# Optimization experiments

Hardware: AMD Instinct MI355X
Metric: run time of the kernel (lower is better)

## Reference

```python
import jax, jax.numpy as jnp
import numpy as np

LOG_VAR_Q = 0.0
TEMPERATURE = 0.5


def setup_inputs() -> dict:
    key = jax.random.key(0)
    k1, k2, k3 = jax.random.split(key, 3)
    bs, dim_z, W, H, K = 64, 64, 32, 32, 1024
    x = jax.random.normal(k1, (bs, dim_z, W, H), dtype=jnp.float32)
    codebook = jax.random.normal(k2, (K, dim_z), dtype=jnp.float32)
    log_var_q_scalar = jnp.asarray(0.0, dtype=jnp.float32)
    # pre-sampled standard Gumbel noise for the relaxed categorical
    u = jax.random.uniform(k3, (bs * W * H, K), dtype=jnp.float32,
                           minval=1e-6, maxval=1.0 - 1e-6)
    gumbel_noise = -jnp.log(-jnp.log(u))
    return {"x": x, "codebook": codebook,
            "log_var_q_scalar": log_var_q_scalar,
            "gumbel_noise": gumbel_noise}


def reference(x, codebook, log_var_q_scalar, gumbel_noise):
    bs, dim_z, W, H = x.shape
    # [bs, dim_z, W, H] -> [bs*W*H, dim_z]
    x_flat = jnp.transpose(x, (0, 2, 3, 1)).reshape(-1, dim_z)

    var_q = jnp.exp(jnp.asarray(LOG_VAR_Q, x.dtype)) + jnp.exp(log_var_q_scalar)
    precision_q = 1.0 / jnp.clip(var_q, 1e-10)
    w = 0.5 * precision_q  # scalar weight on squared distances

    sq_x = jnp.sum(x_flat * x_flat, axis=-1, keepdims=True)
    sq_c = jnp.sum(codebook * codebook, axis=-1)
    cross = jnp.einsum('nd,kd->nk', x_flat, codebook)
    logit = -w * (sq_x - 2.0 * cross + sq_c)

    log_probs = jax.nn.log_softmax(logit, axis=-1)
    probs = jnp.exp(log_probs)

    # gumbel-softmax relaxed one-hot encodings
    encodings = jax.nn.softmax((logit + gumbel_noise) / TEMPERATURE, axis=-1)

    quantized = jnp.einsum('nk,kd->nd', encodings, codebook)
    quantized = jnp.transpose(quantized.reshape(bs, W, H, dim_z), (0, 3, 1, 2))

    kld_discrete = jnp.sum(probs * log_probs) / bs
    kld_continuous = jnp.mean(jnp.sum(w * (x - quantized) ** 2, axis=(1, 2, 3)))
    return quantized, kld_discrete + kld_continuous
```

## Files before the change

### kernel.cpp

```cpp
#include <hip/hip_runtime.h>
#include <math.h>

#define K_CB 1024
#define D_Z  64
#define MT   32
#define NTOT 65536
#define NBLK (NTOT / MT)

typedef __attribute__((ext_vector_type(8)))  short s16x8;
typedef __attribute__((ext_vector_type(4)))  short s16x4;
typedef __attribute__((ext_vector_type(4)))  float f32x4;
typedef __attribute__((ext_vector_type(16))) float f32x16;

#define WS_CB16  0
#define WS_CBT16 131072
#define WS_NWSQC 262144
#define WS_PART  266240

__device__ __forceinline__ unsigned short f2b(float f) {
  unsigned int u = __float_as_uint(f);
  u += 0x7fffu + ((u >> 16) & 1u);
  return (unsigned short)(u >> 16);
}

__global__ void vq_prep(const float* __restrict__ cb, const float* __restrict__ lvq,
                        unsigned char* __restrict__ wsb) {
  unsigned short* cb16  = (unsigned short*)(wsb + WS_CB16);
  unsigned short* cbT16 = (unsigned short*)(wsb + WS_CBT16);
  float* nwsqc = (float*)(wsb + WS_NWSQC);
  const float w = 0.5f / fmaxf(1.0f + __expf(lvq[0]), 1e-10f);
  const int tid = threadIdx.x;
  const int k  = blockIdx.x * 16 + (tid >> 4);
  const int d0 = (tid & 15) * 4;
  const f32x4 v = *(const f32x4*)(cb + k * D_Z + d0);
  s16x4 b4;
  #pragma unroll
  for (int i = 0; i < 4; i++) b4[i] = (short)f2b(v[i]);
  *(s16x4*)(cb16 + k * D_Z + d0) = b4;
  #pragma unroll
  for (int i = 0; i < 4; i++) cbT16[(d0 + i) * K_CB + k] = (unsigned short)b4[i];
  float s = v[0]*v[0] + v[1]*v[1] + v[2]*v[2] + v[3]*v[3];
  #pragma unroll
  for (int off = 1; off < 16; off <<= 1) s += __shfl_xor(s, off);
  if ((tid & 15) == 0) nwsqc[k] = -w * s;
}

__global__ __launch_bounds__(512, 4)
void vq_main(const float* __restrict__ x, const float* __restrict__ gum,
             const float* __restrict__ lvq, unsigned char* __restrict__ wsb,
             float* __restrict__ out) {
  __shared__ __align__(16) unsigned short xa[MT * D_Z];
  __shared__ __align__(16) unsigned short es[MT * K_CB];
  __shared__ __align__(16) float stats[8][MT][4];
  __shared__ __align__(16) float s2s[8][MT];
  __shared__ float kldrow[MT];
  __shared__ float wred[8];

  const int tid  = threadIdx.x;
  const int w    = tid >> 6;
  const int lane = tid & 63;
  const int m32  = lane & 31;
  const int hi   = lane >> 5;
  const int bid  = blockIdx.x;
  const int blk  = ((bid & 7) << 8) | (bid >> 3);
  const int row0 = blk * MT;
  const int bidx = row0 >> 10;
  const int rem0 = row0 & 1023;
  const int kw0  = w << 7;

  const float wq = 0.5f / fmaxf(1.0f + __expf(lvq[0]), 1e-10f);
  const float w2 = 2.0f * wq;

  const unsigned short* cb16  = (const unsigned short*)(wsb + WS_CB16);
  const unsigned short* cbT16 = (const unsigned short*)(wsb + WS_CBT16);
  const float* nwsqc = (const float*)(wsb + WS_NWSQC);

  {
    const int m = tid & 31, dg = tid >> 5;
    #pragma unroll
    for (int i = 0; i < 4; i++) {
      const int d = dg + 16 * i;
      const float v = x[((bidx * D_Z + d) << 10) + rem0 + m];
      xa[(m * D_Z + d) ^ ((m & 7) << 3)] = f2b(v);
    }
  }
  __syncthreads();

  f32x16 acc[4];
  #pragma unroll
  for (int t = 0; t < 4; t++)
    #pragma unroll
    for (int r = 0; r < 16; r++) acc[t][r] = 0.f;
  {
    s16x8 bx[4];
    #pragma unroll
    for (int kb = 0; kb < 4; kb++) {
      const int byteoff = (m32 * 128 + kb * 32 + hi * 16) ^ ((m32 & 7) << 4);
      bx[kb] = *(const s16x8*)((const unsigned char*)xa + byteoff);
    }
    #pragma unroll
    for (int t = 0; t < 4; t++) {
      const unsigned short* ap = cb16 + (kw0 + t * 32 + m32) * D_Z + hi * 8;
      #pragma unroll
      for (int kb = 0; kb < 4; kb++) {
        const s16x8 a = *(const s16x8*)(ap + kb * 16);
        acc[t] = __builtin_amdgcn_mfma_f32_32x32x16_bf16(a, bx[kb], acc[t], 0, 0, 0);
      }
    }
  }

  float m1 = -3.4e38f;
  #pragma unroll
  for (int t = 0; t < 4; t++) {
    #pragma unroll
    for (int q = 0; q < 4; q++) {
      const f32x4 nw = *(const f32x4*)(nwsqc + kw0 + t * 32 + q * 8 + hi * 4);
      #pragma unroll
      for (int i = 0; i < 4; i++) {
        acc[t][q * 4 + i] = fmaf(w2, acc[t][q * 4 + i], nw[i]);
        m1 = fmaxf(m1, acc[t][q * 4 + i]);
      }
    }
  }
  m1 = fmaxf(m1, __shfl_xor(m1, 32));

  const float* gp = gum + ((size_t)(row0 + m32) << 10) + kw0 + hi * 4;
  f32x4 gA[8];
  #pragma unroll
  for (int u = 0; u < 8; u++)
    gA[u] = *(const f32x4*)(gp + (u >> 2) * 32 + (u & 3) * 8);

  float s1 = 0.f, Aa = 0.f;
  #pragma unroll
  for (int t = 0; t < 4; t++) {
    #pragma unroll
    for (int r = 0; r < 16; r++) {
      const float u = acc[t][r] - m1;
      const float e = __expf(u);
      s1 += e;
      Aa = fmaf(u, e, Aa);
    }
  }
  s1 += __shfl_xor(s1, 32);
  Aa += __shfl_xor(Aa, 32);

  float m2 = -3.4e38f;
  #pragma unroll
  for (int u = 0; u < 8; u++) {
    const int t = u >> 2, q = u & 3;
    #pragma unroll
    for (int i = 0; i < 4; i++) {
      const float z = 2.0f * (acc[t][q * 4 + i] + gA[u][i]);
      acc[t][q * 4 + i] = z;
      m2 = fmaxf(m2, z);
    }
  }
  f32x4 gB[8];
  #pragma unroll
  for (int u = 0; u < 8; u++)
    gB[u] = *(const f32x4*)(gp + 64 + (u >> 2) * 32 + (u & 3) * 8);
  #pragma unroll
  for (int u = 0; u < 8; u++) {
    const int t = 2 + (u >> 2), q = u & 3;
    #pragma unroll
    for (int i = 0; i < 4; i++) {
      const float z = 2.0f * (acc[t][q * 4 + i] + gB[u][i]);
      acc[t][q * 4 + i] = z;
      m2 = fmaxf(m2, z);
    }
  }
  m2 = fmaxf(m2, __shfl_xor(m2, 32));
  if (hi == 0) {
    f32x4 st = {m1, s1, Aa, m2};
    *(f32x4*)&stats[w][m32][0] = st;
  }
  __syncthreads();

  float M2 = -3.4e38f;
  {
    f32x4 st[8];
    #pragma unroll
    for (int q = 0; q < 8; q++) {
      st[q] = *(const f32x4*)&stats[q][m32][0];
      M2 = fmaxf(M2, st[q][3]);
    }
    if (w == 0) {
      float M1 = -3.4e38f;
      #pragma unroll
      for (int q = 0; q < 8; q++) M1 = fmaxf(M1, st[q][0]);
      float s1g = 0.f, Ag = 0.f;
      #pragma unroll
      for (int q = 0; q < 8; q++) {
        const float dm = st[q][0] - M1;
        const float c  = __expf(dm);
        s1g += c * st[q][1];
        Ag = fmaf(c, fmaf(dm, st[q][1], st[q][2]), Ag);
      }
      if (hi == 0) kldrow[m32] = Ag / s1g - __logf(s1g);
    }
  }

  float s2 = 0.f;
  #pragma unroll
  for (int t = 0; t < 4; t++) {
    #pragma unroll
    for (int q = 0; q < 4; q++) {
      float e[4];
      #pragma unroll
      for (int i = 0; i < 4; i++) {
        e[i] = __expf(acc[t][q * 4 + i] - M2);
        s2 += e[i];
      }
      const unsigned int p0 = (unsigned int)f2b(e[0]) | ((unsigned int)f2b(e[1]) << 16);
      const unsigned int p1 = (unsigned int)f2b(e[2]) | ((unsigned int)f2b(e[3]) << 16);
      const unsigned long long pk = (unsigned long long)p0 | ((unsigned long long)p1 << 32);
      const int byteoff = (m32 * 2048 + (kw0 + t * 32 + q * 8 + hi * 4) * 2) ^ ((m32 & 7) << 4);
      *(unsigned long long*)((unsigned char*)es + byteoff) = pk;
    }
  }
  s2 += __shfl_xor(s2, 32);
  if (hi == 0) s2s[w][m32] = s2;
  __syncthreads();

  const int m16 = lane & 15, g = lane >> 4;
  const int db = w >> 1, mb = w & 1;
  const int mrow = mb * 16 + m16;
  float s2g = 0.f;
  #pragma unroll
  for (int q = 0; q < 8; q++) s2g += s2s[q][mrow];
  const float inv2 = 1.0f / s2g;

  f32x4 qacc = (f32x4){0.f, 0.f, 0.f, 0.f};
  {
    const unsigned short* a2p = cbT16 + (db * 16 + m16) * K_CB + g * 8;
    const unsigned char* esb = (const unsigned char*)es;
    #pragma unroll
    for (int kc = 0; kc < 32; kc++) {
      const s16x8 a2 = *(const s16x8*)(a2p + kc * 32);
      const int byteoff = (mrow * 2048 + kc * 64 + g * 16) ^ ((m16 & 7) << 4);
      const s16x8 b2 = *(const s16x8*)(esb + byteoff);
      qacc = __builtin_amdgcn_mfma_f32_16x16x32_bf16(a2, b2, qacc, 0, 0, 0);
    }
  }

  float kca = 0.f;
  #pragma unroll
  for (int r = 0; r < 4; r++) {
    const int d = db * 16 + g * 4 + r;
    const int off = ((bidx * D_Z + d) << 10) + rem0 + mrow;
    const float qv = qacc[r] * inv2;
    const float xv = x[off];
    out[off] = qv;
    const float dx = xv - qv;
    kca = fmaf(dx, dx, kca);
  }
  #pragma unroll
  for (int off = 1; off < 64; off <<= 1) kca += __shfl_xor(kca, off);
  if (lane == 0) wred[w] = kca;
  __syncthreads();
  if (tid == 0) {
    float tot = 0.f;
    #pragma unroll
    for (int q = 0; q < 8; q++) tot += wred[q];
    tot *= wq;
    #pragma unroll
    for (int i = 0; i < MT; i++) tot += kldrow[i];
    ((float*)(wsb + WS_PART))[blk] = tot;
  }
}

__global__ void vq_reduce(const unsigned char* __restrict__ wsb, float* __restrict__ out) {
  __shared__ float red[256];
  const float* part = (const float*)(wsb + WS_PART);
  const int t = threadIdx.x;
  float s = 0.f;
  for (int i = t; i < NBLK; i += 256) s += part[i];
  red[t] = s;
  __syncthreads();
  for (int st = 128; st > 0; st >>= 1) {
    if (t < st) red[t] += red[t + st];
    __syncthreads();
  }
  if (t == 0) out[NTOT * D_Z] = red[0] * (1.0f / 64.0f);
}

extern "C" void kernel_launch(void* const* d_in, const int* in_sizes, int n_in,
                              void* d_out, int out_size, void* d_ws, size_t ws_size,
                              hipStream_t stream) {
  const float* x   = (const float*)d_in[0];
  const float* cb  = (const float*)d_in[1];
  const float* lvq = (const float*)d_in[2];
  const float* gum = (const float*)d_in[3];
  float* out = (float*)d_out;
  unsigned char* wsb = (unsigned char*)d_ws;

  hipLaunchKernelGGL(vq_prep,   dim3(64),   dim3(256), 0, stream, cb, lvq, wsb);
  hipLaunchKernelGGL(vq_main,   dim3(NBLK), dim3(512), 0, stream, x, gum, lvq, wsb, out);
  hipLaunchKernelGGL(vq_reduce, dim3(1),    dim3(256), 0, stream, wsb, out);
}
```

Before: 160.5 us.

## Hoist gumbel and codebook loads ahead of MFMAs and double-buffer second GEMM

Moves the gumbel-noise loads and the codebook fragment loads ahead of the first distance MFMAs so global memory latency overlaps with matrix work. The quantize GEMM now double-buffers its codebook-transpose fragments, and the x reads for the KL term are issued before that GEMM. Launch bounds drop from 4 to 2 blocks per SM to leave room for the extra live registers. The trade is lower occupancy in exchange for more loads in flight per wave.

Result: slower. 186.5 us (+16.3%).

```diff
diff --git a/kernel.cpp b/kernel.cpp
--- a/kernel.cpp
+++ b/kernel.cpp
@@ -45,7 +45,7 @@
   if ((tid & 15) == 0) nwsqc[k] = -w * s;
 }
 
-__global__ __launch_bounds__(512, 4)
+__global__ __launch_bounds__(512, 2)
 void vq_main(const float* __restrict__ x, const float* __restrict__ gum,
              const float* __restrict__ lvq, unsigned char* __restrict__ wsb,
              float* __restrict__ out) {
@@ -91,23 +91,31 @@
   for (int t = 0; t < 4; t++)
     #pragma unroll
     for (int r = 0; r < 16; r++) acc[t][r] = 0.f;
-  {
-    s16x8 bx[4];
-    #pragma unroll
-    for (int kb = 0; kb < 4; kb++) {
-      const int byteoff = (m32 * 128 + kb * 32 + hi * 16) ^ ((m32 & 7) << 4);
-      bx[kb] = *(const s16x8*)((const unsigned char*)xa + byteoff);
-    }
-    #pragma unroll
-    for (int t = 0; t < 4; t++) {
-      const unsigned short* ap = cb16 + (kw0 + t * 32 + m32) * D_Z + hi * 8;
-      #pragma unroll
-      for (int kb = 0; kb < 4; kb++) {
-        const s16x8 a = *(const s16x8*)(ap + kb * 16);
-        acc[t] = __builtin_amdgcn_mfma_f32_32x32x16_bf16(a, bx[kb], acc[t], 0, 0, 0);
-      }
-    }
-  }
+
+  const float* gp = gum + ((size_t)(row0 + m32) << 10) + kw0 + hi * 4;
+  const unsigned short* ap = cb16 + (kw0 + m32) * D_Z + hi * 8;
+  f32x4 gA[8], gB[8];
+  s16x8 bx[4], af[8];
+
+  #pragma unroll
+  for (int kb = 0; kb < 4; kb++) {
+    const int byteoff = (m32 * 128 + kb * 32 + hi * 16) ^ ((m32 & 7) << 4);
+    bx[kb] = *(const s16x8*)((const unsigned char*)xa + byteoff);
+  }
+  #pragma unroll
+  for (int i = 0; i < 8; i++) af[i] = *(const s16x8*)(ap + (i >> 2) * 2048 + (i & 3) * 16);
+  #pragma unroll
+  for (int u = 0; u < 8; u++) gA[u] = *(const f32x4*)(gp + (u >> 2) * 32 + (u & 3) * 8);
+  #pragma unroll
+  for (int i = 0; i < 8; i++)
+    acc[i >> 2] = __builtin_amdgcn_mfma_f32_32x32x16_bf16(af[i], bx[i & 3], acc[i >> 2], 0, 0, 0);
+  #pragma unroll
+  for (int i = 0; i < 8; i++) af[i] = *(const s16x8*)(ap + (2 + (i >> 2)) * 2048 + (i & 3) * 16);
+  #pragma unroll
+  for (int u = 0; u < 8; u++) gB[u] = *(const f32x4*)(gp + 64 + (u >> 2) * 32 + (u & 3) * 8);
+  #pragma unroll
+  for (int i = 0; i < 8; i++)
+    acc[2 + (i >> 2)] = __builtin_amdgcn_mfma_f32_32x32x16_bf16(af[i], bx[i & 3], acc[2 + (i >> 2)], 0, 0, 0);
 
   float m1 = -3.4e38f;
   #pragma unroll
@@ -123,12 +131,6 @@
     }
   }
   m1 = fmaxf(m1, __shfl_xor(m1, 32));
-
-  const float* gp = gum + ((size_t)(row0 + m32) << 10) + kw0 + hi * 4;
-  f32x4 gA[8];
-  #pragma unroll
-  for (int u = 0; u < 8; u++)
-    gA[u] = *(const f32x4*)(gp + (u >> 2) * 32 + (u & 3) * 8);
 
   float s1 = 0.f, Aa = 0.f;
   #pragma unroll
@@ -155,10 +157,6 @@
       m2 = fmaxf(m2, z);
     }
   }
-  f32x4 gB[8];
-  #pragma unroll
-  for (int u = 0; u < 8; u++)
-    gB[u] = *(const f32x4*)(gp + 64 + (u >> 2) * 32 + (u & 3) * 8);
   #pragma unroll
   for (int u = 0; u < 8; u++) {
     const int t = 2 + (u >> 2), q = u & 3;
@@ -230,28 +228,45 @@
   for (int q = 0; q < 8; q++) s2g += s2s[q][mrow];
   const float inv2 = 1.0f / s2g;
 
+  int offs[4];
+  float xv[4];
+  #pragma unroll
+  for (int r = 0; r < 4; r++) {
+    const int d = db * 16 + g * 4 + r;
+    offs[r] = ((bidx * D_Z + d) << 10) + rem0 + mrow;
+    xv[r] = x[offs[r]];
+  }
+
   f32x4 qacc = (f32x4){0.f, 0.f, 0.f, 0.f};
   {
     const unsigned short* a2p = cbT16 + (db * 16 + m16) * K_CB + g * 8;
     const unsigned char* esb = (const unsigned char*)es;
-    #pragma unroll
-    for (int kc = 0; kc < 32; kc++) {
-      const s16x8 a2 = *(const s16x8*)(a2p + kc * 32);
-      const int byteoff = (mrow * 2048 + kc * 64 + g * 16) ^ ((m16 & 7) << 4);
-      const s16x8 b2 = *(const s16x8*)(esb + byteoff);
-      qacc = __builtin_amdgcn_mfma_f32_16x16x32_bf16(a2, b2, qacc, 0, 0, 0);
+    s16x8 a2b[2][4];
+    #pragma unroll
+    for (int j = 0; j < 4; j++) a2b[0][j] = *(const s16x8*)(a2p + j * 32);
+    #pragma unroll
+    for (int c = 0; c < 8; c++) {
+      if (c < 7) {
+        #pragma unroll
+        for (int j = 0; j < 4; j++)
+          a2b[(c + 1) & 1][j] = *(const s16x8*)(a2p + ((c + 1) * 4 + j) * 32);
+      }
+      #pragma unroll
+      for (int j = 0; j < 4; j++) {
+        const int kc = c * 4 + j;
+        const int byteoff = (mrow * 2048 + kc * 64 + g * 16) ^ ((m16 & 7) << 4);
+        const s16x8 b2 = *(const s16x8*)(esb + byteoff);
+        qacc = __builtin_amdgcn_mfma_f32_16x16x32_bf16(a2b[c & 1][j], b2, qacc, 0, 0, 0);
+      }
     }
   }
 
   float kca = 0.f;
   #pragma unroll
   for (int r = 0; r < 4; r++) {
-    const int d = db * 16 + g * 4 + r;
-    const int off = ((bidx * D_Z + d) << 10) + rem0 + mrow;
     const float qv = qacc[r] * inv2;
-    const float xv = x[off];
-    out[off] = qv;
-    const float dx = xv - qv;
+    out[offs[r]] = qv;
+    const float dx = xv[r] - qv;
     kca = fmaf(dx, dx, kca);
   }
   #pragma unroll
```

## Prefetch gumbel noise before MFMA and fuse final reduction via last-block atomic

Applied to the files above, without the earlier changes.

All the Gumbel noise for each thread's tile is now loaded, pre-doubled, before the barrier and the codebook matmul, so the global load latency overlaps with computing the distances. The separate reduction kernel is removed: each block increments an atomic counter after writing its partial sum, and the last block to finish sums all partials, which saves one kernel launch. Launch bounds drop from 4 to 3 blocks per SM to make room for the extra 64 registers of prefetched noise. The cost is lower occupancy and a serial tail reduction done in the last block.

New measurement: 261.9 us. 1.63x slower.

```diff
diff --git a/kernel.cpp b/kernel.cpp
--- a/kernel.cpp
+++ b/kernel.cpp
@@ -16,6 +16,7 @@
 #define WS_CBT16 131072
 #define WS_NWSQC 262144
 #define WS_PART  266240
+#define WS_CNT   274432
 
 __device__ __forceinline__ unsigned short f2b(float f) {
   unsigned int u = __float_as_uint(f);
@@ -30,6 +31,7 @@
   float* nwsqc = (float*)(wsb + WS_NWSQC);
   const float w = 0.5f / fmaxf(1.0f + __expf(lvq[0]), 1e-10f);
   const int tid = threadIdx.x;
+  if (blockIdx.x == 0 && tid == 0) *(int*)(wsb + WS_CNT) = 0;
   const int k  = blockIdx.x * 16 + (tid >> 4);
   const int d0 = (tid & 15) * 4;
   const f32x4 v = *(const f32x4*)(cb + k * D_Z + d0);
@@ -45,7 +47,7 @@
   if ((tid & 15) == 0) nwsqc[k] = -w * s;
 }
 
-__global__ __launch_bounds__(512, 4)
+__global__ __launch_bounds__(512, 3)
 void vq_main(const float* __restrict__ x, const float* __restrict__ gum,
              const float* __restrict__ lvq, unsigned char* __restrict__ wsb,
              float* __restrict__ out) {
@@ -55,6 +57,7 @@
   __shared__ __align__(16) float s2s[8][MT];
   __shared__ float kldrow[MT];
   __shared__ float wred[8];
+  __shared__ int lastf;
 
   const int tid  = threadIdx.x;
   const int w    = tid >> 6;
@@ -84,6 +87,14 @@
       xa[(m * D_Z + d) ^ ((m & 7) << 3)] = f2b(v);
     }
   }
+
+  const float* gp = gum + ((size_t)(row0 + m32) << 10) + kw0 + hi * 4;
+  f32x4 h[16];
+  #pragma unroll
+  for (int u = 0; u < 16; u++) {
+    const f32x4 v = *(const f32x4*)(gp + (u >> 2) * 32 + (u & 3) * 8);
+    h[u] = v + v;
+  }
   __syncthreads();
 
   f32x16 acc[4];
@@ -123,12 +134,6 @@
     }
   }
   m1 = fmaxf(m1, __shfl_xor(m1, 32));
-
-  const float* gp = gum + ((size_t)(row0 + m32) << 10) + kw0 + hi * 4;
-  f32x4 gA[8];
-  #pragma unroll
-  for (int u = 0; u < 8; u++)
-    gA[u] = *(const f32x4*)(gp + (u >> 2) * 32 + (u & 3) * 8);
 
   float s1 = 0.f, Aa = 0.f;
   #pragma unroll
@@ -146,25 +151,11 @@
 
   float m2 = -3.4e38f;
   #pragma unroll
-  for (int u = 0; u < 8; u++) {
+  for (int u = 0; u < 16; u++) {
     const int t = u >> 2, q = u & 3;
     #pragma unroll
     for (int i = 0; i < 4; i++) {
-      const float z = 2.0f * (acc[t][q * 4 + i] + gA[u][i]);
-      acc[t][q * 4 + i] = z;
-      m2 = fmaxf(m2, z);
-    }
-  }
-  f32x4 gB[8];
-  #pragma unroll
-  for (int u = 0; u < 8; u++)
-    gB[u] = *(const f32x4*)(gp + 64 + (u >> 2) * 32 + (u & 3) * 8);
-  #pragma unroll
-  for (int u = 0; u < 8; u++) {
-    const int t = 2 + (u >> 2), q = u & 3;
-    #pragma unroll
-    for (int i = 0; i < 4; i++) {
-      const float z = 2.0f * (acc[t][q * 4 + i] + gB[u][i]);
+      const float z = fmaf(2.0f, acc[t][q * 4 + i], h[u][i]);
       acc[t][q * 4 + i] = z;
       m2 = fmaxf(m2, z);
     }
@@ -266,22 +257,29 @@
     #pragma unroll
     for (int i = 0; i < MT; i++) tot += kldrow[i];
     ((float*)(wsb + WS_PART))[blk] = tot;
-  }
-}
-
-__global__ void vq_reduce(const unsigned char* __restrict__ wsb, float* __restrict__ out) {
-  __shared__ float red[256];
-  const float* part = (const float*)(wsb + WS_PART);
-  const int t = threadIdx.x;
-  float s = 0.f;
-  for (int i = t; i < NBLK; i += 256) s += part[i];
-  red[t] = s;
-  __syncthreads();
-  for (int st = 128; st > 0; st >>= 1) {
-    if (t < st) red[t] += red[t + st];
+    __threadfence();
+    const int old = atomicAdd((int*)(wsb + WS_CNT), 1);
+    lastf = (old == NBLK - 1);
+  }
+  __syncthreads();
+
+  if (lastf) {
+    __threadfence();
+    const float* part = (const float*)(wsb + WS_PART);
+    float s = 0.f;
+    #pragma unroll
+    for (int i = 0; i < NBLK / 512; i++) s += part[tid + i * 512];
+    #pragma unroll
+    for (int off = 1; off < 64; off <<= 1) s += __shfl_xor(s, off);
+    if (lane == 0) wred[w] = s;
     __syncthreads();
-  }
-  if (t == 0) out[NTOT * D_Z] = red[0] * (1.0f / 64.0f);
+    if (tid == 0) {
+      float t2 = 0.f;
+      #pragma unroll
+      for (int q = 0; q < 8; q++) t2 += wred[q];
+      out[NTOT * D_Z] = t2 * (1.0f / 64.0f);
+    }
+  }
 }
 
 extern "C" void kernel_launch(void* const* d_in, const int* in_sizes, int n_in,
@@ -294,7 +292,6 @@
   float* out = (float*)d_out;
   unsigned char* wsb = (unsigned char*)d_ws;
 
-  hipLaunchKernelGGL(vq_prep,   dim3(64),   dim3(256), 0, stream, cb, lvq, wsb);
-  hipLaunchKernelGGL(vq_main,   dim3(NBLK), dim3(512), 0, stream, x, gum, lvq, wsb, out);
-  hipLaunchKernelGGL(vq_reduce, dim3(1),    dim3(256), 0, stream, wsb, out);
-}
+  hipLaunchKernelGGL(vq_prep, dim3(64),   dim3(256), 0, stream, cb, lvq, wsb);
+  hipLaunchKernelGGL(vq_main, dim3(NBLK), dim3(512), 0, stream, x, gum, lvq, wsb, out);
+}
```
